# Kernel tuning notes

Measured on AMD Instinct MI355X. Metric: run time of the kernel, lower is better.

The kernel has to match this reference:

```python
import jax, jax.numpy as jnp
import numpy as np
import math

DIM = 256
NUM_HEADS = 8
WS = 7  # window side (7x7 windows)


def setup_inputs() -> dict:
    key = jax.random.key(0)
    ks = jax.random.split(key, 7)
    B, H, W, C = 32, 56, 56, DIM
    x = jax.random.normal(ks[0], (B, H, W, C), dtype=jnp.float32)
    s = 1.0 / math.sqrt(C)
    Wq = jax.random.normal(ks[1], (C, C), dtype=jnp.float32) * s
    bq = jax.random.normal(ks[2], (C,), dtype=jnp.float32) * 0.01
    Wk = jax.random.normal(ks[3], (C, C), dtype=jnp.float32) * s
    bk = jax.random.normal(ks[4], (C,), dtype=jnp.float32) * 0.01
    Wv = jax.random.normal(ks[5], (C, C), dtype=jnp.float32) * s
    bv = jax.random.normal(ks[6], (C,), dtype=jnp.float32) * 0.01
    return {"x": x, "Wq": Wq, "bq": bq, "Wk": Wk, "bk": bk, "Wv": Wv, "bv": bv}


def _window_partition(x):
    # [B, H, W, C] -> [B, nW, WS*WS, C]
    B, H, W, C = x.shape
    x = x.reshape(B, H // WS, WS, W // WS, WS, C)
    x = x.transpose(0, 1, 3, 2, 4, 5)
    return x.reshape(B, (H // WS) * (W // WS), WS * WS, C)


def reference(x, Wq, bq, Wk, bk, Wv, bv):
    B, H, W, C = x.shape
    hd = C // NUM_HEADS
    win = _window_partition(x)              # [B, nW, T, C], T = 49
    nW, T = win.shape[1], win.shape[2]

    def proj(Wm, bm):
        # nn.Linear: y = x @ W^T + b; split heads -> [B, nW, T, h, hd]
        y = jnp.einsum('bwtc,dc->bwtd', win, Wm) + bm
        return y.reshape(B, nW, T, NUM_HEADS, hd)

    q = proj(Wq, bq)
    k = proj(Wk, bk)
    v = proj(Wv, bv)

    # NOTE: original scales by sqrt(self.dimension) (full dim), not head_dim.
    scale = 1.0 / math.sqrt(C)
    logits = jnp.einsum('bwqhd,bwkhd->bwhqk', q, k) * scale  # [B, nW, h, T, T]
    attn = jax.nn.softmax(logits, axis=-1)
    out = jnp.einsum('bwhqk,bwkhd->bwqhd', attn, v)          # [B, nW, T, h, hd]
    return out.reshape(B, nW, T, C)
```

## Files before the change

kernel.cpp:

```cpp
#include <hip/hip_runtime.h>
#include <hip/hip_bf16.h>

typedef __bf16 bf16_t;
typedef __bf16 bf16x8 __attribute__((ext_vector_type(8)));
typedef float  f32x4  __attribute__((ext_vector_type(4)));

#define XP 264
#define QP 72
#define VP 72
#define PP 72
#define SCL 0.09016844f

__device__ inline bf16x8 cvt8(f32x4 a, f32x4 b) {
    bf16x8 r;
    r[0]=(bf16_t)a[0]; r[1]=(bf16_t)a[1]; r[2]=(bf16_t)a[2]; r[3]=(bf16_t)a[3];
    r[4]=(bf16_t)b[0]; r[5]=(bf16_t)b[1]; r[6]=(bf16_t)b[2]; r[7]=(bf16_t)b[3];
    return r;
}

__global__ __launch_bounds__(256)
void wcvt_kernel(const float* __restrict__ Wq, const float* __restrict__ Wk,
                 const float* __restrict__ Wv, bf16_t* __restrict__ o)
{
    int e = (blockIdx.x * 256 + threadIdx.x) * 8;
    const float* src = (e < 65536) ? (Wq + e)
                     : (e < 131072 ? (Wk + (e - 65536)) : (Wv + (e - 131072)));
    f32x4 f0 = *(const f32x4*)src;
    f32x4 f1 = *(const f32x4*)(src + 4);
    *(bf16x8*)(o + e) = cvt8(f0, f1);
}

__global__ __launch_bounds__(256, 3)
void swin_win_attn(const float* __restrict__ x,
                   const bf16_t* __restrict__ Wb,
                   const float* __restrict__ bq, const float* __restrict__ bk,
                   const float* __restrict__ bv,
                   float* __restrict__ out)
{
    __shared__ __attribute__((aligned(16))) bf16_t smem[49 * XP + 2 * 64 * QP + 64 * VP];
    bf16_t* sX  = smem;
    bf16_t* sQ  = smem + 49 * XP;
    bf16_t* sK  = sQ + 64 * QP;
    bf16_t* sVT = sK + 64 * QP;

    const int tid  = threadIdx.x;
    const int wv   = tid >> 6;
    const int lane = tid & 63;
    const int l15  = lane & 15;
    const int quad = lane >> 4;

    const int bid = blockIdx.x;
    const int win = ((bid >> 5) << 3) | (bid & 7);
    const int g   = (bid >> 3) & 3;

    const int b  = win >> 6;
    const int w  = win & 63;
    const int wy = w >> 3;
    const int wx = w & 7;
    const float* xw = x + (((b * 56) + wy * 7) * 56 + wx * 7) * 256;

    f32x4 la[7], lb[7];
    #pragma unroll
    for (int k = 0; k < 6; ++k) {
        int idx = k * 256 + tid, row = idx >> 5, cv = idx & 31;
        int ty = row / 7, tx = row - ty * 7;
        const float* src = xw + (ty * 56 + tx) * 256 + cv * 8;
        la[k] = *(const f32x4*)src;
        lb[k] = *(const f32x4*)(src + 4);
    }
    if (tid < 32) {
        const float* src = xw + (6 * 56 + 6) * 256 + tid * 8;
        la[6] = *(const f32x4*)src;
        lb[6] = *(const f32x4*)(src + 4);
    }
    #pragma unroll
    for (int k = 0; k < 6; ++k) {
        int idx = k * 256 + tid, row = idx >> 5, cv = idx & 31;
        *(bf16x8*)&sX[row * XP + cv * 8] = cvt8(la[k], lb[k]);
    }
    if (tid < 32)
        *(bf16x8*)&sX[48 * XP + tid * 8] = cvt8(la[6], lb[6]);

    const int dglob = g * 64 + wv * 16 + l15;
    const int lcol  = wv * 16 + l15;
    const bf16_t* wbase = Wb + dglob * 256 + quad * 8;
    bf16x8 wq[8];
    #pragma unroll
    for (int ks = 0; ks < 8; ++ks) wq[ks] = *(const bf16x8*)(wbase + ks * 32);
    const float biq = bq[dglob], bik = bk[dglob], biv = bv[dglob];
    __syncthreads();

    {
        f32x4 acc[4];
        #pragma unroll
        for (int mt = 0; mt < 4; ++mt) acc[mt] = f32x4{0.f, 0.f, 0.f, 0.f};
        #pragma unroll
        for (int ks = 0; ks < 8; ++ks) {
            #pragma unroll
            for (int mt = 0; mt < 4; ++mt) {
                bf16x8 a = *(const bf16x8*)&sX[(mt * 16 + l15) * XP + ks * 32 + quad * 8];
                acc[mt] = __builtin_amdgcn_mfma_f32_16x16x32_bf16(a, wq[ks], acc[mt], 0, 0, 0);
            }
        }
        #pragma unroll
        for (int mt = 0; mt < 4; ++mt)
            #pragma unroll
            for (int r = 0; r < 4; ++r) {
                int row = mt * 16 + quad * 4 + r;
                sQ[row * QP + lcol] = (bf16_t)(acc[mt][r] + biq);
            }
    }
    {
        bf16x8 wt[8];
        #pragma unroll
        for (int ks = 0; ks < 8; ++ks) wt[ks] = *(const bf16x8*)(wbase + 2 * 65536 + ks * 32);
        f32x4 acc[4];
        #pragma unroll
        for (int mt = 0; mt < 4; ++mt) acc[mt] = f32x4{0.f, 0.f, 0.f, 0.f};
        #pragma unroll
        for (int ks = 0; ks < 8; ++ks) {
            #pragma unroll
            for (int mt = 0; mt < 4; ++mt) {
                bf16x8 a = *(const bf16x8*)&sX[(mt * 16 + l15) * XP + ks * 32 + quad * 8];
                acc[mt] = __builtin_amdgcn_mfma_f32_16x16x32_bf16(a, wt[ks], acc[mt], 0, 0, 0);
            }
        }
        #pragma unroll
        for (int mt = 0; mt < 4; ++mt)
            #pragma unroll
            for (int r = 0; r < 4; ++r) {
                int row = mt * 16 + quad * 4 + r;
                sVT[lcol * VP + row] = (row < 49) ? (bf16_t)(acc[mt][r] + biv) : (bf16_t)0.0f;
            }
    }
    {
        bf16x8 wt[8];
        #pragma unroll
        for (int ks = 0; ks < 8; ++ks) wt[ks] = *(const bf16x8*)(wbase + 65536 + ks * 32);
        f32x4 acc[4];
        #pragma unroll
        for (int mt = 0; mt < 4; ++mt) acc[mt] = f32x4{0.f, 0.f, 0.f, 0.f};
        #pragma unroll
        for (int ks = 0; ks < 8; ++ks) {
            #pragma unroll
            for (int mt = 0; mt < 4; ++mt) {
                bf16x8 a = *(const bf16x8*)&sX[(mt * 16 + l15) * XP + ks * 32 + quad * 8];
                acc[mt] = __builtin_amdgcn_mfma_f32_16x16x32_bf16(a, wt[ks], acc[mt], 0, 0, 0);
            }
        }
        #pragma unroll
        for (int mt = 0; mt < 4; ++mt)
            #pragma unroll
            for (int r = 0; r < 4; ++r) {
                int row = mt * 16 + quad * 4 + r;
                sK[row * QP + lcol] = (bf16_t)(acc[mt][r] + bik);
            }
    }
    __syncthreads();

    bf16_t* sP = &sX[wv * 16 * PP];
    bf16x8 vone;
    #pragma unroll
    for (int j = 0; j < 8; ++j) vone[j] = (bf16_t)1.0f;

    #pragma unroll
    for (int hs = 0; hs < 2; ++hs) {
        const int hc = hs * 32;
        bf16x8 aq = *(const bf16x8*)&sQ[(wv * 16 + l15) * QP + hc + quad * 8];
        f32x4 sc[4];
        #pragma unroll
        for (int tj = 0; tj < 4; ++tj) {
            bf16x8 kb = *(const bf16x8*)&sK[(tj * 16 + l15) * QP + hc + quad * 8];
            f32x4 z = {0.f, 0.f, 0.f, 0.f};
            sc[tj] = __builtin_amdgcn_mfma_f32_16x16x32_bf16(aq, kb, z, 0, 0, 0);
        }
        #pragma unroll
        for (int r = 0; r < 4; ++r) {
            float p0 = __builtin_amdgcn_exp2f(sc[0][r] * SCL);
            float p1 = __builtin_amdgcn_exp2f(sc[1][r] * SCL);
            float p2 = __builtin_amdgcn_exp2f(sc[2][r] * SCL);
            float p3 = (l15 == 0) ? __builtin_amdgcn_exp2f(sc[3][r] * SCL) : 0.0f;
            int pr = (quad * 4 + r) * PP;
            sP[pr + l15]      = (bf16_t)p0;
            sP[pr + 16 + l15] = (bf16_t)p1;
            sP[pr + 32 + l15] = (bf16_t)p2;
            sP[pr + 48 + l15] = (bf16_t)p3;
        }
        f32x4 o0 = {0.f,0.f,0.f,0.f}, o1 = {0.f,0.f,0.f,0.f}, lsum = {0.f,0.f,0.f,0.f};
        #pragma unroll
        for (int ks = 0; ks < 2; ++ks) {
            bf16x8 ap = *(const bf16x8*)&sP[l15 * PP + ks * 32 + quad * 8];
            bf16x8 b0 = *(const bf16x8*)&sVT[(hc + l15) * VP + ks * 32 + quad * 8];
            bf16x8 b1 = *(const bf16x8*)&sVT[(hc + 16 + l15) * VP + ks * 32 + quad * 8];
            o0   = __builtin_amdgcn_mfma_f32_16x16x32_bf16(ap, b0,   o0,   0, 0, 0);
            o1   = __builtin_amdgcn_mfma_f32_16x16x32_bf16(ap, b1,   o1,   0, 0, 0);
            lsum = __builtin_amdgcn_mfma_f32_16x16x32_bf16(ap, vone, lsum, 0, 0, 0);
        }
        const int h = g * 2 + hs;
        #pragma unroll
        for (int r = 0; r < 4; ++r) {
            int t = wv * 16 + quad * 4 + r;
            if (t < 49) {
                float rinv = __builtin_amdgcn_rcpf(lsum[r]);
                long off = (long)(win * 49 + t) * 256 + h * 32 + l15;
                out[off]      = o0[r] * rinv;
                out[off + 16] = o1[r] * rinv;
            }
        }
    }
}

extern "C" void kernel_launch(void* const* d_in, const int* in_sizes, int n_in,
                              void* d_out, int out_size, void* d_ws, size_t ws_size,
                              hipStream_t stream) {
    const float* x  = (const float*)d_in[0];
    const float* Wq = (const float*)d_in[1];
    const float* bq = (const float*)d_in[2];
    const float* Wk = (const float*)d_in[3];
    const float* bk = (const float*)d_in[4];
    const float* Wv = (const float*)d_in[5];
    const float* bv = (const float*)d_in[6];
    float* out = (float*)d_out;
    bf16_t* Wb = (bf16_t*)d_ws;
    (void)in_sizes; (void)n_in; (void)out_size; (void)ws_size;

    hipLaunchKernelGGL(wcvt_kernel, dim3(96), dim3(256), 0, stream, Wq, Wk, Wv, Wb);
    hipLaunchKernelGGL(swin_win_attn, dim3(8192), dim3(256), 0, stream,
                       x, Wb, bq, bk, bv, out);
}
```

Before: 272.4 us.

## Process all four head groups per window in one block, loading x once

Each block now handles a whole window and loops over the four 64-column head groups. Before, four separate blocks each reloaded the same window of x from global memory. The rows of sX that get overwritten by the P scratch are saved in registers and written back before the next group. This cuts x global reads fourfold and the grid shrinks from 8192 to 2048 blocks. In exchange there are more registers, extra barriers, serial per-block work, and less parallelism to hide latency.

```diff
diff --git a/kernel.cpp b/kernel.cpp
--- a/kernel.cpp
+++ b/kernel.cpp
@@ -49,10 +49,7 @@
     const int l15  = lane & 15;
     const int quad = lane >> 4;
 
-    const int bid = blockIdx.x;
-    const int win = ((bid >> 5) << 3) | (bid & 7);
-    const int g   = (bid >> 3) & 3;
-
+    const int win = blockIdx.x;
     const int b  = win >> 6;
     const int w  = win & 63;
     const int wy = w >> 3;
@@ -73,139 +70,168 @@
         la[6] = *(const f32x4*)src;
         lb[6] = *(const f32x4*)(src + 4);
     }
+    bf16x8 xreg[3];
     #pragma unroll
     for (int k = 0; k < 6; ++k) {
         int idx = k * 256 + tid, row = idx >> 5, cv = idx & 31;
-        *(bf16x8*)&sX[row * XP + cv * 8] = cvt8(la[k], lb[k]);
+        bf16x8 c = cvt8(la[k], lb[k]);
+        if (k < 3) xreg[k] = c;
+        *(bf16x8*)&sX[row * XP + cv * 8] = c;
     }
     if (tid < 32)
         *(bf16x8*)&sX[48 * XP + tid * 8] = cvt8(la[6], lb[6]);
 
-    const int dglob = g * 64 + wv * 16 + l15;
-    const int lcol  = wv * 16 + l15;
+    const int lcol = wv * 16 + l15;
+    int dglob = lcol;
     const bf16_t* wbase = Wb + dglob * 256 + quad * 8;
     bf16x8 wq[8];
     #pragma unroll
     for (int ks = 0; ks < 8; ++ks) wq[ks] = *(const bf16x8*)(wbase + ks * 32);
-    const float biq = bq[dglob], bik = bk[dglob], biv = bv[dglob];
+    float biq = bq[dglob], bik = bk[dglob], biv = bv[dglob];
+
+    bf16x8 vone;
+    #pragma unroll
+    for (int j = 0; j < 8; ++j) vone[j] = (bf16_t)1.0f;
+
     __syncthreads();
 
-    {
-        f32x4 acc[4];
+    #pragma unroll 1
+    for (int g = 0; g < 4; ++g) {
+        {
+            f32x4 acc[4];
+            #pragma unroll
+            for (int mt = 0; mt < 4; ++mt) acc[mt] = f32x4{0.f, 0.f, 0.f, 0.f};
+            #pragma unroll
+            for (int ks = 0; ks < 8; ++ks) {
+                #pragma unroll
+                for (int mt = 0; mt < 4; ++mt) {
+                    bf16x8 a = *(const bf16x8*)&sX[(mt * 16 + l15) * XP + ks * 32 + quad * 8];
+                    acc[mt] = __builtin_amdgcn_mfma_f32_16x16x32_bf16(a, wq[ks], acc[mt], 0, 0, 0);
+                }
+            }
+            #pragma unroll
+            for (int mt = 0; mt < 4; ++mt)
+                #pragma unroll
+                for (int r = 0; r < 4; ++r) {
+                    int row = mt * 16 + quad * 4 + r;
+                    sQ[row * QP + lcol] = (bf16_t)(acc[mt][r] + biq);
+                }
+        }
+        {
+            bf16x8 wt[8];
+            #pragma unroll
+            for (int ks = 0; ks < 8; ++ks) wt[ks] = *(const bf16x8*)(wbase + 2 * 65536 + ks * 32);
+            f32x4 acc[4];
+            #pragma unroll
+            for (int mt = 0; mt < 4; ++mt) acc[mt] = f32x4{0.f, 0.f, 0.f, 0.f};
+            #pragma unroll
+            for (int ks = 0; ks < 8; ++ks) {
+                #pragma unroll
+                for (int mt = 0; mt < 4; ++mt) {
+                    bf16x8 a = *(const bf16x8*)&sX[(mt * 16 + l15) * XP + ks * 32 + quad * 8];
+                    acc[mt] = __builtin_amdgcn_mfma_f32_16x16x32_bf16(a, wt[ks], acc[mt], 0, 0, 0);
+                }
+            }
+            #pragma unroll
+            for (int mt = 0; mt < 4; ++mt)
+                #pragma unroll
+                for (int r = 0; r < 4; ++r) {
+                    int row = mt * 16 + quad * 4 + r;
+                    sVT[lcol * VP + row] = (row < 49) ? (bf16_t)(acc[mt][r] + biv) : (bf16_t)0.0f;
+                }
+        }
+        {
+            bf16x8 wt[8];
+            #pragma unroll
+            for (int ks = 0; ks < 8; ++ks) wt[ks] = *(const bf16x8*)(wbase + 65536 + ks * 32);
+            f32x4 acc[4];
+            #pragma unroll
+            for (int mt = 0; mt < 4; ++mt) acc[mt] = f32x4{0.f, 0.f, 0.f, 0.f};
+            #pragma unroll
+            for (int ks = 0; ks < 8; ++ks) {
+                #pragma unroll
+                for (int mt = 0; mt < 4; ++mt) {
+                    bf16x8 a = *(const bf16x8*)&sX[(mt * 16 + l15) * XP + ks * 32 + quad * 8];
+                    acc[mt] = __builtin_amdgcn_mfma_f32_16x16x32_bf16(a, wt[ks], acc[mt], 0, 0, 0);
+                }
+            }
+            #pragma unroll
+            for (int mt = 0; mt < 4; ++mt)
+                #pragma unroll
+                for (int r = 0; r < 4; ++r) {
+                    int row = mt * 16 + quad * 4 + r;
+                    sK[row * QP + lcol] = (bf16_t)(acc[mt][r] + bik);
+                }
+        }
+        __syncthreads();
+
+        bf16_t* sP = &sX[wv * 16 * PP];
         #pragma unroll
-        for (int mt = 0; mt < 4; ++mt) acc[mt] = f32x4{0.f, 0.f, 0.f, 0.f};
-        #pragma unroll
-        for (int ks = 0; ks < 8; ++ks) {
-            #pragma unroll
-            for (int mt = 0; mt < 4; ++mt) {
-                bf16x8 a = *(const bf16x8*)&sX[(mt * 16 + l15) * XP + ks * 32 + quad * 8];
-                acc[mt] = __builtin_amdgcn_mfma_f32_16x16x32_bf16(a, wq[ks], acc[mt], 0, 0, 0);
-            }
-        }
-        #pragma unroll
-        for (int mt = 0; mt < 4; ++mt)
+        for (int hs = 0; hs < 2; ++hs) {
+            const int hc = hs * 32;
+            bf16x8 aq = *(const bf16x8*)&sQ[(wv * 16 + l15) * QP + hc + quad * 8];
+            f32x4 sc[4];
+            #pragma unroll
+            for (int tj = 0; tj < 4; ++tj) {
+                bf16x8 kb = *(const bf16x8*)&sK[(tj * 16 + l15) * QP + hc + quad * 8];
+                f32x4 z = {0.f, 0.f, 0.f, 0.f};
+                sc[tj] = __builtin_amdgcn_mfma_f32_16x16x32_bf16(aq, kb, z, 0, 0, 0);
+            }
             #pragma unroll
             for (int r = 0; r < 4; ++r) {
-                int row = mt * 16 + quad * 4 + r;
-                sQ[row * QP + lcol] = (bf16_t)(acc[mt][r] + biq);
-            }
-    }
-    {
-        bf16x8 wt[8];
-        #pragma unroll
-        for (int ks = 0; ks < 8; ++ks) wt[ks] = *(const bf16x8*)(wbase + 2 * 65536 + ks * 32);
-        f32x4 acc[4];
-        #pragma unroll
-        for (int mt = 0; mt < 4; ++mt) acc[mt] = f32x4{0.f, 0.f, 0.f, 0.f};
-        #pragma unroll
-        for (int ks = 0; ks < 8; ++ks) {
-            #pragma unroll
-            for (int mt = 0; mt < 4; ++mt) {
-                bf16x8 a = *(const bf16x8*)&sX[(mt * 16 + l15) * XP + ks * 32 + quad * 8];
-                acc[mt] = __builtin_amdgcn_mfma_f32_16x16x32_bf16(a, wt[ks], acc[mt], 0, 0, 0);
-            }
-        }
-        #pragma unroll
-        for (int mt = 0; mt < 4; ++mt)
+                float p0 = __builtin_amdgcn_exp2f(sc[0][r] * SCL);
+                float p1 = __builtin_amdgcn_exp2f(sc[1][r] * SCL);
+                float p2 = __builtin_amdgcn_exp2f(sc[2][r] * SCL);
+                float p3 = (l15 == 0) ? __builtin_amdgcn_exp2f(sc[3][r] * SCL) : 0.0f;
+                int pr = (quad * 4 + r) * PP;
+                sP[pr + l15]      = (bf16_t)p0;
+                sP[pr + 16 + l15] = (bf16_t)p1;
+                sP[pr + 32 + l15] = (bf16_t)p2;
+                sP[pr + 48 + l15] = (bf16_t)p3;
+            }
+            f32x4 o0 = {0.f,0.f,0.f,0.f}, o1 = {0.f,0.f,0.f,0.f}, lsum = {0.f,0.f,0.f,0.f};
+            #pragma unroll
+            for (int ks = 0; ks < 2; ++ks) {
+                bf16x8 ap = *(const bf16x8*)&sP[l15 * PP + ks * 32 + quad * 8];
+                bf16x8 b0 = *(const bf16x8*)&sVT[(hc + l15) * VP + ks * 32 + quad * 8];
+                bf16x8 b1 = *(const bf16x8*)&sVT[(hc + 16 + l15) * VP + ks * 32 + quad * 8];
+                o0   = __builtin_amdgcn_mfma_f32_16x16x32_bf16(ap, b0,   o0,   0, 0, 0);
+                o1   = __builtin_amdgcn_mfma_f32_16x16x32_bf16(ap, b1,   o1,   0, 0, 0);
+                lsum = __builtin_amdgcn_mfma_f32_16x16x32_bf16(ap, vone, lsum, 0, 0, 0);
+            }
+            const int h = g * 2 + hs;
             #pragma unroll
             for (int r = 0; r < 4; ++r) {
-                int row = mt * 16 + quad * 4 + r;
-                sVT[lcol * VP + row] = (row < 49) ? (bf16_t)(acc[mt][r] + biv) : (bf16_t)0.0f;
-            }
-    }
-    {
-        bf16x8 wt[8];
-        #pragma unroll
-        for (int ks = 0; ks < 8; ++ks) wt[ks] = *(const bf16x8*)(wbase + 65536 + ks * 32);
-        f32x4 acc[4];
-        #pragma unroll
-        for (int mt = 0; mt < 4; ++mt) acc[mt] = f32x4{0.f, 0.f, 0.f, 0.f};
-        #pragma unroll
-        for (int ks = 0; ks < 8; ++ks) {
-            #pragma unroll
-            for (int mt = 0; mt < 4; ++mt) {
-                bf16x8 a = *(const bf16x8*)&sX[(mt * 16 + l15) * XP + ks * 32 + quad * 8];
-                acc[mt] = __builtin_amdgcn_mfma_f32_16x16x32_bf16(a, wt[ks], acc[mt], 0, 0, 0);
-            }
-        }
-        #pragma unroll
-        for (int mt = 0; mt < 4; ++mt)
-            #pragma unroll
-            for (int r = 0; r < 4; ++r) {
-                int row = mt * 16 + quad * 4 + r;
-                sK[row * QP + lcol] = (bf16_t)(acc[mt][r] + bik);
-            }
-    }
-    __syncthreads();
-
-    bf16_t* sP = &sX[wv * 16 * PP];
-    bf16x8 vone;
-    #pragma unroll
-    for (int j = 0; j < 8; ++j) vone[j] = (bf16_t)1.0f;
-
-    #pragma unroll
-    for (int hs = 0; hs < 2; ++hs) {
-        const int hc = hs * 32;
-        bf16x8 aq = *(const bf16x8*)&sQ[(wv * 16 + l15) * QP + hc + quad * 8];
-        f32x4 sc[4];
-        #pragma unroll
-        for (int tj = 0; tj < 4; ++tj) {
-            bf16x8 kb = *(const bf16x8*)&sK[(tj * 16 + l15) * QP + hc + quad * 8];
-            f32x4 z = {0.f, 0.f, 0.f, 0.f};
-            sc[tj] = __builtin_amdgcn_mfma_f32_16x16x32_bf16(aq, kb, z, 0, 0, 0);
-        }
-        #pragma unroll
-        for (int r = 0; r < 4; ++r) {
-            float p0 = __builtin_amdgcn_exp2f(sc[0][r] * SCL);
-            float p1 = __builtin_amdgcn_exp2f(sc[1][r] * SCL);
-            float p2 = __builtin_amdgcn_exp2f(sc[2][r] * SCL);
-            float p3 = (l15 == 0) ? __builtin_amdgcn_exp2f(sc[3][r] * SCL) : 0.0f;
-            int pr = (quad * 4 + r) * PP;
-            sP[pr + l15]      = (bf16_t)p0;
-            sP[pr + 16 + l15] = (bf16_t)p1;
-            sP[pr + 32 + l15] = (bf16_t)p2;
-            sP[pr + 48 + l15] = (bf16_t)p3;
-        }
-        f32x4 o0 = {0.f,0.f,0.f,0.f}, o1 = {0.f,0.f,0.f,0.f}, lsum = {0.f,0.f,0.f,0.f};
-        #pragma unroll
-        for (int ks = 0; ks < 2; ++ks) {
-            bf16x8 ap = *(const bf16x8*)&sP[l15 * PP + ks * 32 + quad * 8];
-            bf16x8 b0 = *(const bf16x8*)&sVT[(hc + l15) * VP + ks * 32 + quad * 8];
-            bf16x8 b1 = *(const bf16x8*)&sVT[(hc + 16 + l15) * VP + ks * 32 + quad * 8];
-            o0   = __builtin_amdgcn_mfma_f32_16x16x32_bf16(ap, b0,   o0,   0, 0, 0);
-            o1   = __builtin_amdgcn_mfma_f32_16x16x32_bf16(ap, b1,   o1,   0, 0, 0);
-            lsum = __builtin_amdgcn_mfma_f32_16x16x32_bf16(ap, vone, lsum, 0, 0, 0);
-        }
-        const int h = g * 2 + hs;
-        #pragma unroll
-        for (int r = 0; r < 4; ++r) {
-            int t = wv * 16 + quad * 4 + r;
-            if (t < 49) {
-                float rinv = __builtin_amdgcn_rcpf(lsum[r]);
-                long off = (long)(win * 49 + t) * 256 + h * 32 + l15;
-                out[off]      = o0[r] * rinv;
-                out[off + 16] = o1[r] * rinv;
-            }
+                int t = wv * 16 + quad * 4 + r;
+                if (t < 49) {
+                    float rinv = __builtin_amdgcn_rcpf(lsum[r]);
+                    long off = (long)(win * 49 + t) * 256 + h * 32 + l15;
+                    out[off]      = o0[r] * rinv;
+                    out[off + 16] = o1[r] * rinv;
+                }
+            }
+        }
+        __syncthreads();
+
+        if (g < 3) {
+            {
+                int row = tid >> 5, cv = tid & 31;
+                *(bf16x8*)&sX[row * XP + cv * 8] = xreg[0];
+            }
+            {
+                int idx = 256 + tid, row = idx >> 5, cv = idx & 31;
+                *(bf16x8*)&sX[row * XP + cv * 8] = xreg[1];
+            }
+            if (tid < 64) {
+                int row = 16 + (tid >> 5), cv = tid & 31;
+                *(bf16x8*)&sX[row * XP + cv * 8] = xreg[2];
+            }
+            dglob += 64;
+            wbase += 64 * 256;
+            #pragma unroll
+            for (int ks = 0; ks < 8; ++ks) wq[ks] = *(const bf16x8*)(wbase + ks * 32);
+            biq = bq[dglob]; bik = bk[dglob]; biv = bv[dglob];
+            __syncthreads();
         }
     }
 }
@@ -225,6 +251,6 @@
     (void)in_sizes; (void)n_in; (void)out_size; (void)ws_size;
 
     hipLaunchKernelGGL(wcvt_kernel, dim3(96), dim3(256), 0, stream, Wq, Wk, Wv, Wb);
-    hipLaunchKernelGGL(swin_win_attn, dim3(8192), dim3(256), 0, stream,
+    hipLaunchKernelGGL(swin_win_attn, dim3(2048), dim3(256), 0, stream,
                        x, Wb, bq, bk, bv, out);
 }
```

New measurement: 292.5 us. 7.4% more time.
